# Optimization experiments

Hardware: AMD Instinct MI355X
Metric: run time of the kernel (lower is better)

Reference implementation:

```python
import jax, jax.numpy as jnp
import numpy as np

B, D, N = 2, 64, 512          # batch, channel dim, flattened spatial tokens
H = 4 * D                     # hidden_dim default = input_dim * 4
OUT = D                       # output_dim default = input_dim


def setup_inputs() -> dict:
    key = jax.random.key(0)
    ks = jax.random.split(key, 11)
    s = 0.02
    inp = {
        "input": jax.random.normal(ks[0], (B, D, N), dtype=jnp.float32),
        # inner MLP: Linear(2D->H), ReLU, Linear(H->H), ReLU, Linear(H->H)
        "w1": jax.random.normal(ks[1], (2 * D, H), dtype=jnp.float32) * s,
        "b1": jnp.zeros((H,), jnp.float32),
        "w2": jax.random.normal(ks[2], (H, H), dtype=jnp.float32) * s,
        "b2": jnp.zeros((H,), jnp.float32),
        "w3": jax.random.normal(ks[3], (H, H), dtype=jnp.float32) * s,
        "b3": jnp.zeros((H,), jnp.float32),
        # outer MLP: Linear(H->H), ReLU, Linear(H->OUT)
        "w4": jax.random.normal(ks[4], (H, H), dtype=jnp.float32) * s,
        "b4": jnp.zeros((H,), jnp.float32),
        "w5": jax.random.normal(ks[5], (H, OUT), dtype=jnp.float32) * s,
        "b5": jnp.zeros((OUT,), jnp.float32),
    }
    return inp


def reference(input, w1, b1, w2, b2, w3, b3, w4, b4, w5, b5):
    # channels-first -> channels-last, flatten spatial: [B, N, D]
    x = jnp.transpose(input, (0, 2, 1))
    d = x.shape[-1]
    # pairs[b, c, i] = concat(x[b, i], x[b, c]); decompose first linear:
    # pairs @ w1 = x_i @ w1[:D] + x_c @ w1[D:], avoiding the [B,N,N,2D] cat tensor.
    hi = x @ w1[:d]   # input part, indexed by dim 2 -> [B, N, H]
    hc = x @ w1[d:]   # context part, indexed by dim 1 -> [B, N, H]
    h = jax.nn.relu(hi[:, None, :, :] + hc[:, :, None, :] + b1)  # [B, N, N, H]
    h = jax.nn.relu(h @ w2 + b2)
    h = h @ w3 + b3
    mid = h.sum(axis=(1, 2))              # sum(1).sum(1) -> [B, H]; mid nonlinearity = Identity
    o = jax.nn.relu(mid @ w4 + b4)
    return o @ w5 + b5                     # [B, OUT]
```

## Files before the change

### kernel.cpp

```cpp
#include <hip/hip_runtime.h>


using f32x16  = __attribute__((ext_vector_type(16))) float;
using short8  = __attribute__((ext_vector_type(8))) short;
using float4v = __attribute__((ext_vector_type(4))) float;

__device__ __forceinline__ short f2bf(float f) {
    unsigned u = __float_as_uint(f);
    unsigned r = u + 0x7FFFu + ((u >> 16) & 1u);
    return (short)(r >> 16);
}

__device__ __forceinline__ short8 relu_pack8(float4v lo, float4v hi4) {
#pragma unroll
    for (int e = 0; e < 4; ++e) {
        lo[e]  = fmaxf(lo[e], 0.f);
        hi4[e] = fmaxf(hi4[e], 0.f);
    }
    union { short8 s; unsigned u[4]; } r;
    asm("v_cvt_pk_bf16_f32 %0, %1, %2" : "=v"(r.u[0]) : "v"(lo[0]),  "v"(lo[1]));
    asm("v_cvt_pk_bf16_f32 %0, %1, %2" : "=v"(r.u[1]) : "v"(lo[2]),  "v"(lo[3]));
    asm("v_cvt_pk_bf16_f32 %0, %1, %2" : "=v"(r.u[2]) : "v"(hi4[0]), "v"(hi4[1]));
    asm("v_cvt_pk_bf16_f32 %0, %1, %2" : "=v"(r.u[3]) : "v"(hi4[2]), "v"(hi4[3]));
    return r.s;
}

__global__ __launch_bounds__(256) void prep(const float* __restrict__ in,
                                            const float* __restrict__ w1,
                                            const float* __restrict__ b1,
                                            const float* __restrict__ w2,
                                            float* __restrict__ hi,
                                            float* __restrict__ hcb,
                                            short* __restrict__ bfrag) {
    int tid = threadIdx.x;
    int bidx = blockIdx.x;
    if (bidx < 256) {
        int b = bidx >> 7, n0 = (bidx & 127) * 4;
        __shared__ float xs[4][64];
        {
            int nn = tid >> 6, d = tid & 63;
            xs[nn][d] = in[(size_t)(b * 64 + d) * 512 + n0 + nn];
        }
        __syncthreads();
        float a0[4] = {0.f, 0.f, 0.f, 0.f}, a1[4] = {0.f, 0.f, 0.f, 0.f};
#pragma unroll 8
        for (int d = 0; d < 64; ++d) {
            float wA = w1[d * 256 + tid];
            float wB = w1[(64 + d) * 256 + tid];
#pragma unroll
            for (int nn = 0; nn < 4; ++nn) {
                a0[nn] += xs[nn][d] * wA;
                a1[nn] += xs[nn][d] * wB;
            }
        }
        float bb = b1[tid];
#pragma unroll
        for (int nn = 0; nn < 4; ++nn) {
            size_t o = (size_t)(b * 512 + n0 + nn) * 256 + tid;
            hi[o]  = a0[nn];
            hcb[o] = a1[nn] + bb;
        }
    } else {
        int idx = (bidx - 256) * 256 + tid;
        int k = idx >> 8, ncol = idx & 255;
        int n = ncol >> 5, col = ncol & 31;
        int kk = k >> 4, h = (k >> 3) & 1, j = k & 7;
        int off = (((n * 16 + kk) * 64) + h * 32 + col) * 8 + j;
        bfrag[off] = f2bf(w2[k * 256 + ncol]);
    }
}

__global__ __launch_bounds__(512, 1) void big(const float* __restrict__ hi_,
                                              const float* __restrict__ hcb_,
                                              const short8* __restrict__ bfrag,
                                              const float* __restrict__ b2,
                                              float* __restrict__ partials) {
    __shared__ __align__(16) short8 ring[6][1024];
    __shared__ unsigned ready_f[6];
    __shared__ unsigned done_f[6];

    const int tid = threadIdx.x;
    const int bid = blockIdx.x;
    const int b = bid >> 7, cq = bid & 127;

    if (tid < 6) { ready_f[tid] = 0u; done_f[tid] = 4u; }
    __syncthreads();

    volatile unsigned* vready = ready_f;
    volatile unsigned* vdone  = done_f;

    const int w = tid >> 6, lane = tid & 63;
    const int l31 = lane & 31, h = lane >> 5;

    if (w < 4) {
        short8 bfr0[16], bfr1[16];
#pragma unroll
        for (int kk = 0; kk < 16; ++kk) {
            bfr0[kk] = bfrag[(size_t)((w * 16 + kk) * 64 + lane)];
            bfr1[kk] = bfrag[(size_t)(((w + 4) * 16 + kk) * 64 + lane)];
        }
        const float b2v0 = b2[w * 32 + l31];
        const float b2v1 = b2[(w + 4) * 32 + l31];
        float js0 = 0.f, js1 = 0.f;

#pragma unroll 1
        for (int t = 0; t < 64; ++t) {
            const int s = t % 6;
            while (vready[s] != (unsigned)(t + 1)) __builtin_amdgcn_s_sleep(1);
            const short8* __restrict__ slot = &ring[s][lane];

            f32x16 aA0, aA1, aB0, aB1;
#pragma unroll
            for (int e = 0; e < 16; ++e) { aA0[e] = 0.f; aA1[e] = 0.f; aB0[e] = 0.f; aB1[e] = 0.f; }

            __builtin_amdgcn_s_setprio(1);
#pragma unroll
            for (int kk = 0; kk < 16; kk += 2) {
                short8 a0 = slot[kk * 64];
                short8 a1 = slot[(kk + 1) * 64];
                aA0 = __builtin_amdgcn_mfma_f32_32x32x16_bf16(a0, bfr0[kk],     aA0, 0, 0, 0);
                aB0 = __builtin_amdgcn_mfma_f32_32x32x16_bf16(a0, bfr1[kk],     aB0, 0, 0, 0);
                aA1 = __builtin_amdgcn_mfma_f32_32x32x16_bf16(a1, bfr0[kk + 1], aA1, 0, 0, 0);
                aB1 = __builtin_amdgcn_mfma_f32_32x32x16_bf16(a1, bfr1[kk + 1], aB1, 0, 0, 0);
            }
            __builtin_amdgcn_s_setprio(0);
            if (lane == 0) atomicAdd(&done_f[s], 1u);

            float s0a = 0.f, s0b = 0.f, s1a = 0.f, s1b = 0.f;
#pragma unroll
            for (int e = 0; e < 16; e += 2) {
                s0a += fmaxf(aA0[e]     + aA1[e]     + b2v0, 0.f);
                s0b += fmaxf(aA0[e + 1] + aA1[e + 1] + b2v0, 0.f);
                s1a += fmaxf(aB0[e]     + aB1[e]     + b2v1, 0.f);
                s1b += fmaxf(aB0[e + 1] + aB1[e + 1] + b2v1, 0.f);
            }
            js0 += s0a + s0b;
            js1 += s1a + s1b;
        }
        js0 += __shfl_xor(js0, 32);
        js1 += __shfl_xor(js1, 32);
        if (h == 0) {
            partials[((size_t)(b * 256 + w * 32 + l31)) * 128 + cq]       = js0;
            partials[((size_t)(b * 256 + (w + 4) * 32 + l31)) * 128 + cq] = js1;
        }
    } else {
        const int pw = w - 4;
        const int ip = l31 & 7, cq4 = l31 >> 3;
        const float* __restrict__ hrowb = hi_ + (size_t)b * 131072
                                        + (size_t)ip * 256 + h * 8;
        const float* __restrict__ crow  = hcb_ + (size_t)b * 131072
                                        + (size_t)(cq * 4 + cq4) * 256 + h * 8;
#pragma unroll 1
        for (int t = pw; t < 64; t += 4) {
            const int s = t % 6;
            while (vdone[s] != 4u) __builtin_amdgcn_s_sleep(1);
            if (lane == 0) vdone[s] = 0u;
            const float* __restrict__ hrow = hrowb + (size_t)t * (8 * 256);
            short8* __restrict__ slot = &ring[s][lane];
#pragma unroll
            for (int kk = 0; kk < 16; ++kk) {
                float4v x0 = *reinterpret_cast<const float4v*>(hrow + kk * 16);
                float4v x1 = *reinterpret_cast<const float4v*>(hrow + kk * 16 + 4);
                float4v c0 = *reinterpret_cast<const float4v*>(crow + kk * 16);
                float4v c1 = *reinterpret_cast<const float4v*>(crow + kk * 16 + 4);
                slot[kk * 64] = relu_pack8(x0 + c0, x1 + c1);
            }
            asm volatile("s_waitcnt lgkmcnt(0)" ::: "memory");
            if (lane == 0) vready[s] = (unsigned)(t + 1);
        }
    }
}

__global__ __launch_bounds__(128) void reduceK(const float* __restrict__ partials,
                                               float* __restrict__ su_g) {
    int tid = threadIdx.x, blk = blockIdx.x;
    float s = partials[(size_t)blk * 128 + tid];
#pragma unroll
    for (int d = 1; d < 64; d <<= 1) s += __shfl_xor(s, d);
    __shared__ float ws[2];
    if ((tid & 63) == 0) ws[tid >> 6] = s;
    __syncthreads();
    if (tid == 0) su_g[blk] = ws[0] + ws[1];
}

__global__ __launch_bounds__(512) void finalK(const float* __restrict__ su_g,
                                              const float* __restrict__ w3,
                                              const float* __restrict__ b3,
                                              const float* __restrict__ w4,
                                              const float* __restrict__ b4,
                                              const float* __restrict__ w5,
                                              const float* __restrict__ b5,
                                              float* __restrict__ out) {
    __shared__ float su[2][256], mid[2][256], o[2][256];
    int tid = threadIdx.x;
    int b = tid >> 8, c = tid & 255;
    su[b][c] = su_g[b * 256 + c];
    __syncthreads();
    float m = 262144.0f * b3[c];
    for (int k = 0; k < 256; ++k) m += su[b][k] * w3[k * 256 + c];
    mid[b][c] = m;
    __syncthreads();
    float ov = b4[c];
    for (int k = 0; k < 256; ++k) ov += mid[b][k] * w4[k * 256 + c];
    o[b][c] = fmaxf(ov, 0.f);
    __syncthreads();
    if (c < 64) {
        float rr = b5[c];
        for (int k = 0; k < 256; ++k) rr += o[b][k] * w5[k * 64 + c];
        out[b * 64 + c] = rr;
    }
}

extern "C" void kernel_launch(void* const* d_in, const int* in_sizes, int n_in,
                              void* d_out, int out_size, void* d_ws, size_t ws_size,
                              hipStream_t stream) {
    const float* in = (const float*)d_in[0];
    const float* w1 = (const float*)d_in[1];
    const float* b1 = (const float*)d_in[2];
    const float* w2 = (const float*)d_in[3];
    const float* b2 = (const float*)d_in[4];
    const float* w3 = (const float*)d_in[5];
    const float* b3 = (const float*)d_in[6];
    const float* w4 = (const float*)d_in[7];
    const float* b4 = (const float*)d_in[8];
    const float* w5 = (const float*)d_in[9];
    const float* b5 = (const float*)d_in[10];
    float* out = (float*)d_out;

    char* ws = (char*)d_ws;
    float* hi       = (float*)(ws);
    float* hcb      = (float*)(ws + (1u << 20));
    short* bfrag    = (short*)(ws + (2u << 20));
    float* partials = (float*)(ws + (2u << 20) + (1u << 18));
    float* su_g     = (float*)(ws + (2u << 20) + (2u << 18));

    prep<<<512, 256, 0, stream>>>(in, w1, b1, w2, hi, hcb, bfrag);
    big<<<256, 512, 0, stream>>>(hi, hcb, (const short8*)bfrag, b2, partials);
    reduceK<<<512, 128, 0, stream>>>(partials, su_g);
    finalK<<<1, 512, 0, stream>>>(su_g, w3, b3, w4, b4, w5, b5, out);
}
```

Measured before the change: 102.5 us.

## Switch layer-2 MFMA from 32x32x16 to 16x16x32 tiles with matching fragment layouts

Replaces the 32x32x16 bf16 MFMA tiles in the consumer waves with 16x16x32 tiles. The w2 fragment packing and the producer's LDS ring write pattern are both rearranged to fit the new operand layout. Bias b2 is now preloaded into the accumulators instead of added afterwards, and the epilogue reduces over smaller 4-wide accumulators with an extra cross-lane shuffle. The aim is shorter MFMA dependency chains and fewer accumulator registers. The cost is more MFMA instructions and a scattered LDS write pattern on the producer side that may cause bank conflicts.

```diff
diff --git a/kernel.cpp b/kernel.cpp
--- a/kernel.cpp
+++ b/kernel.cpp
@@ -1,7 +1,7 @@
 #include <hip/hip_runtime.h>
 
 
-using f32x16  = __attribute__((ext_vector_type(16))) float;
+using f32x4   = __attribute__((ext_vector_type(4))) float;
 using short8  = __attribute__((ext_vector_type(8))) short;
 using float4v = __attribute__((ext_vector_type(4))) float;
 
@@ -63,9 +63,10 @@
     } else {
         int idx = (bidx - 256) * 256 + tid;
         int k = idx >> 8, ncol = idx & 255;
-        int n = ncol >> 5, col = ncol & 31;
-        int kk = k >> 4, h = (k >> 3) & 1, j = k & 7;
-        int off = (((n * 16 + kk) * 64) + h * 32 + col) * 8 + j;
+        int ct = ncol >> 4, lcol = ncol & 15;
+        int q = k >> 5, kg = (k >> 3) & 3, j = k & 7;
+        int lane = lcol + 16 * kg;
+        int off = ((ct * 8 + q) * 64 + lane) * 8 + j;
         bfrag[off] = f2bf(w2[k * 256 + ncol]);
     }
 }
@@ -93,15 +94,17 @@
     const int l31 = lane & 31, h = lane >> 5;
 
     if (w < 4) {
-        short8 bfr0[16], bfr1[16];
-#pragma unroll
-        for (int kk = 0; kk < 16; ++kk) {
-            bfr0[kk] = bfrag[(size_t)((w * 16 + kk) * 64 + lane)];
-            bfr1[kk] = bfrag[(size_t)(((w + 4) * 16 + kk) * 64 + lane)];
-        }
-        const float b2v0 = b2[w * 32 + l31];
-        const float b2v1 = b2[(w + 4) * 32 + l31];
-        float js0 = 0.f, js1 = 0.f;
+        const int cts[4] = {2 * w, 2 * w + 1, 2 * w + 8, 2 * w + 9};
+        short8 bfr[4][8];
+#pragma unroll
+        for (int c = 0; c < 4; ++c)
+#pragma unroll
+            for (int q = 0; q < 8; ++q)
+                bfr[c][q] = bfrag[(size_t)((cts[c] * 8 + q) * 64 + lane)];
+        float b2v[4];
+#pragma unroll
+        for (int c = 0; c < 4; ++c) b2v[c] = b2[cts[c] * 16 + (lane & 15)];
+        float js[4] = {0.f, 0.f, 0.f, 0.f};
 
 #pragma unroll 1
         for (int t = 0; t < 64; ++t) {
@@ -109,39 +112,47 @@
             while (vready[s] != (unsigned)(t + 1)) __builtin_amdgcn_s_sleep(1);
             const short8* __restrict__ slot = &ring[s][lane];
 
-            f32x16 aA0, aA1, aB0, aB1;
-#pragma unroll
-            for (int e = 0; e < 16; ++e) { aA0[e] = 0.f; aA1[e] = 0.f; aB0[e] = 0.f; aB1[e] = 0.f; }
+            f32x4 acc[2][4];
+#pragma unroll
+            for (int rb = 0; rb < 2; ++rb)
+#pragma unroll
+                for (int c = 0; c < 4; ++c)
+#pragma unroll
+                    for (int e = 0; e < 4; ++e) acc[rb][c][e] = b2v[c];
 
             __builtin_amdgcn_s_setprio(1);
 #pragma unroll
-            for (int kk = 0; kk < 16; kk += 2) {
-                short8 a0 = slot[kk * 64];
-                short8 a1 = slot[(kk + 1) * 64];
-                aA0 = __builtin_amdgcn_mfma_f32_32x32x16_bf16(a0, bfr0[kk],     aA0, 0, 0, 0);
-                aB0 = __builtin_amdgcn_mfma_f32_32x32x16_bf16(a0, bfr1[kk],     aB0, 0, 0, 0);
-                aA1 = __builtin_amdgcn_mfma_f32_32x32x16_bf16(a1, bfr0[kk + 1], aA1, 0, 0, 0);
-                aB1 = __builtin_amdgcn_mfma_f32_32x32x16_bf16(a1, bfr1[kk + 1], aB1, 0, 0, 0);
+            for (int q = 0; q < 8; ++q) {
+                short8 a0 = slot[q * 64];
+                short8 a1 = slot[(8 + q) * 64];
+#pragma unroll
+                for (int c = 0; c < 4; ++c) {
+                    acc[0][c] = __builtin_amdgcn_mfma_f32_16x16x32_bf16(a0, bfr[c][q], acc[0][c], 0, 0, 0);
+                    acc[1][c] = __builtin_amdgcn_mfma_f32_16x16x32_bf16(a1, bfr[c][q], acc[1][c], 0, 0, 0);
+                }
             }
             __builtin_amdgcn_s_setprio(0);
             if (lane == 0) atomicAdd(&done_f[s], 1u);
 
-            float s0a = 0.f, s0b = 0.f, s1a = 0.f, s1b = 0.f;
-#pragma unroll
-            for (int e = 0; e < 16; e += 2) {
-                s0a += fmaxf(aA0[e]     + aA1[e]     + b2v0, 0.f);
-                s0b += fmaxf(aA0[e + 1] + aA1[e + 1] + b2v0, 0.f);
-                s1a += fmaxf(aB0[e]     + aB1[e]     + b2v1, 0.f);
-                s1b += fmaxf(aB0[e + 1] + aB1[e + 1] + b2v1, 0.f);
-            }
-            js0 += s0a + s0b;
-            js1 += s1a + s1b;
-        }
-        js0 += __shfl_xor(js0, 32);
-        js1 += __shfl_xor(js1, 32);
-        if (h == 0) {
-            partials[((size_t)(b * 256 + w * 32 + l31)) * 128 + cq]       = js0;
-            partials[((size_t)(b * 256 + (w + 4) * 32 + l31)) * 128 + cq] = js1;
+            float sa = 0.f, sb = 0.f, sc = 0.f, sd = 0.f;
+#pragma unroll
+            for (int e = 0; e < 4; ++e) {
+                sa += fmaxf(acc[0][0][e], 0.f) + fmaxf(acc[1][0][e], 0.f);
+                sb += fmaxf(acc[0][1][e], 0.f) + fmaxf(acc[1][1][e], 0.f);
+                sc += fmaxf(acc[0][2][e], 0.f) + fmaxf(acc[1][2][e], 0.f);
+                sd += fmaxf(acc[0][3][e], 0.f) + fmaxf(acc[1][3][e], 0.f);
+            }
+            js[0] += sa; js[1] += sb; js[2] += sc; js[3] += sd;
+        }
+#pragma unroll
+        for (int c = 0; c < 4; ++c) {
+            js[c] += __shfl_xor(js[c], 16);
+            js[c] += __shfl_xor(js[c], 32);
+        }
+        if (lane < 16) {
+#pragma unroll
+            for (int c = 0; c < 4; ++c)
+                partials[((size_t)(b * 256 + cts[c] * 16 + lane)) * 128 + cq] = js[c];
         }
     } else {
         const int pw = w - 4;
@@ -150,20 +161,21 @@
                                         + (size_t)ip * 256 + h * 8;
         const float* __restrict__ crow  = hcb_ + (size_t)b * 131072
                                         + (size_t)(cq * 4 + cq4) * 256 + h * 8;
+        const int wbase = (l31 >> 4) * 512 + (l31 & 15) + 16 * h;
 #pragma unroll 1
         for (int t = pw; t < 64; t += 4) {
             const int s = t % 6;
             while (vdone[s] != 4u) __builtin_amdgcn_s_sleep(1);
             if (lane == 0) vdone[s] = 0u;
             const float* __restrict__ hrow = hrowb + (size_t)t * (8 * 256);
-            short8* __restrict__ slot = &ring[s][lane];
+            short8* __restrict__ slot = &ring[s][0];
 #pragma unroll
             for (int kk = 0; kk < 16; ++kk) {
                 float4v x0 = *reinterpret_cast<const float4v*>(hrow + kk * 16);
                 float4v x1 = *reinterpret_cast<const float4v*>(hrow + kk * 16 + 4);
                 float4v c0 = *reinterpret_cast<const float4v*>(crow + kk * 16);
                 float4v c1 = *reinterpret_cast<const float4v*>(crow + kk * 16 + 4);
-                slot[kk * 64] = relu_pack8(x0 + c0, x1 + c1);
+                slot[wbase + (kk >> 1) * 64 + (kk & 1) * 32] = relu_pack8(x0 + c0, x1 + c1);
             }
             asm volatile("s_waitcnt lgkmcnt(0)" ::: "memory");
             if (lane == 0) vready[s] = (unsigned)(t + 1);
```

Result: no change. 102.5 us (+0.0%).
